# Kernel optimization log

Measured on AMD Instinct MI355X. Metric: run time of the kernel, lower is better.

The kernel has to match this reference:

```python
import jax, jax.numpy as jnp
import numpy as np

N_NODES = 100000
N_EDGES = 3200000
HIDDEN = 64
OUT = 1


def setup_inputs() -> dict:
    key = jax.random.key(0)
    k_z, k_e, k_w1, k_b1, k_w2, k_b2 = jax.random.split(key, 6)
    z = jax.random.normal(k_z, (N_NODES, HIDDEN), dtype=jnp.float32)
    edge_index = jax.random.randint(k_e, (2, N_EDGES), 0, N_NODES, dtype=jnp.int64)
    # torch Linear default init: U(-1/sqrt(fan_in), 1/sqrt(fan_in))
    lim1 = 1.0 / np.sqrt(2 * HIDDEN)
    lim2 = 1.0 / np.sqrt(HIDDEN)
    W1 = jax.random.uniform(k_w1, (2 * HIDDEN, HIDDEN), jnp.float32, -lim1, lim1)
    b1 = jax.random.uniform(k_b1, (HIDDEN,), jnp.float32, -lim1, lim1)
    W2 = jax.random.uniform(k_w2, (HIDDEN, OUT), jnp.float32, -lim2, lim2)
    b2 = jax.random.uniform(k_b2, (OUT,), jnp.float32, -lim2, lim2)
    return {"z": z, "edge_index": edge_index, "W1": W1, "b1": b1, "W2": W2, "b2": b2}


def reference(z, edge_index, W1, b1, W2, b2):
    row, col = edge_index[0], edge_index[1]
    # gather + concat: [E, 2*HIDDEN]
    h = jnp.concatenate([z[row], z[col]], axis=-1)
    h = jax.nn.relu(h @ W1 + b1)   # [E, HIDDEN]
    out = h @ W2 + b2              # [E, OUT]
    return out
```

## Files before the change

### kernel.cpp

```cpp
#include <hip/hip_runtime.h>
#include <hip/hip_bf16.h>

#define HID 64

__device__ __forceinline__ float bf2f(unsigned short x) {
    return __uint_as_float(((unsigned int)x) << 16);
}

__device__ __forceinline__ unsigned short f2bf(float f) {
    unsigned int u = __float_as_uint(f);
    unsigned int r = (u + 0x7FFFu + ((u >> 16) & 1u)) >> 16;
    return (unsigned short)r;
}

__global__ __launch_bounds__(256) void node_proj_kernel(
    const float* __restrict__ z, const float* __restrict__ W1,
    const float* __restrict__ b1,
    unsigned short* __restrict__ A, unsigned short* __restrict__ B,
    int n_nodes)
{
    const int tid    = blockIdx.x * blockDim.x + threadIdx.x;
    const int lane   = tid & 63;
    const int wave   = tid >> 6;
    const int nwaves = (gridDim.x * blockDim.x) >> 6;
    const int half   = wave & 1;
    const int pair   = wave >> 1;
    const int npairs = nwaves >> 1;

    float w[HID];
#pragma unroll
    for (int k = 0; k < HID; ++k)
        w[k] = W1[(half * HID + k) * HID + lane];
    const float bias = half ? b1[lane] : 0.0f;
    unsigned short* __restrict__ dst = half ? B : A;

    for (int n = pair; n < n_nodes; n += npairs) {
        const int nu = __builtin_amdgcn_readfirstlane(n);
        const float* __restrict__ zr = z + (size_t)nu * HID;
        float a0 = bias, a1 = 0.f, a2 = 0.f, a3 = 0.f;
#pragma unroll
        for (int k4 = 0; k4 < HID / 4; ++k4) {
            a0 = fmaf(zr[4 * k4 + 0], w[4 * k4 + 0], a0);
            a1 = fmaf(zr[4 * k4 + 1], w[4 * k4 + 1], a1);
            a2 = fmaf(zr[4 * k4 + 2], w[4 * k4 + 2], a2);
            a3 = fmaf(zr[4 * k4 + 3], w[4 * k4 + 3], a3);
        }
        dst[(size_t)nu * HID + lane] = f2bf((a0 + a1) + (a2 + a3));
    }
}

__global__ __launch_bounds__(256) void edge_kernel(
    const int* __restrict__ row, const int* __restrict__ col,
    const unsigned short* __restrict__ A, const unsigned short* __restrict__ B,
    const float* __restrict__ W2, const float* __restrict__ b2,
    float* __restrict__ out, int E)
{
    const int tid    = blockIdx.x * blockDim.x + threadIdx.x;
    const int lane   = tid & 63;
    const int gwave  = tid >> 6;
    const int nwaves = (gridDim.x * blockDim.x) >> 6;
    const int sub    = lane >> 3;
    const int l8     = lane & 7;

    float w2r[8];
#pragma unroll
    for (int i = 0; i < 8; ++i) w2r[i] = W2[l8 * 8 + i];
    const float b2v = b2[0];

    const int nchunks = E >> 6;
    for (int ch = gwave; ch < nchunks; ch += nwaves) {
        const int ebase = ch << 6;
        const int r = row[ebase + lane];
        const int c = col[ebase + lane];

        uint4 av[8], bv[8];
#pragma unroll
        for (int g = 0; g < 8; ++g) {
            const int ri = __shfl(r, g * 8 + sub);
            const int ci = __shfl(c, g * 8 + sub);
            av[g] = *(const uint4*)(A + (size_t)ri * HID + l8 * 8);
            bv[g] = *(const uint4*)(B + (size_t)ci * HID + l8 * 8);
        }

#pragma unroll
        for (int g = 0; g < 8; ++g) {
            const unsigned int* au = (const unsigned int*)&av[g];
            const unsigned int* bu = (const unsigned int*)&bv[g];
            float acc = 0.f;
#pragma unroll
            for (int i = 0; i < 4; ++i) {
                float alo = __uint_as_float(au[i] << 16);
                float ahi = __uint_as_float(au[i] & 0xffff0000u);
                float blo = __uint_as_float(bu[i] << 16);
                float bhi = __uint_as_float(bu[i] & 0xffff0000u);
                float slo = fmaxf(alo + blo, 0.f);
                float shi = fmaxf(ahi + bhi, 0.f);
                acc = fmaf(slo, w2r[2 * i + 0], acc);
                acc = fmaf(shi, w2r[2 * i + 1], acc);
            }
            acc += __shfl_xor(acc, 4);
            acc += __shfl_xor(acc, 2);
            acc += __shfl_xor(acc, 1);
            if (l8 == 0) out[ebase + g * 8 + sub] = acc + b2v;
        }
    }
}

extern "C" void kernel_launch(void* const* d_in, const int* in_sizes, int n_in,
                              void* d_out, int out_size, void* d_ws, size_t ws_size,
                              hipStream_t stream) {
    const float* z  = (const float*)d_in[0];
    const int*   ei = (const int*)d_in[1];
    const float* W1 = (const float*)d_in[2];
    const float* b1 = (const float*)d_in[3];
    const float* W2 = (const float*)d_in[4];
    const float* b2 = (const float*)d_in[5];
    float* out = (float*)d_out;

    const int n_nodes = in_sizes[0] / HID;
    const int E       = in_sizes[1] / 2;
    const int* row = ei;
    const int* col = ei + E;

    unsigned short* A = (unsigned short*)d_ws;
    unsigned short* B = A + (size_t)n_nodes * HID;

    node_proj_kernel<<<2048, 256, 0, stream>>>(z, W1, b1, A, B, n_nodes);
    edge_kernel<<<2048, 256, 0, stream>>>(row, col, A, B, W2, b2, out, E);
}
```

Measured before the change: 235.9 us.

## Restructure node projection: node-per-lane with LDS-staged z and transposed W1

```diff
diff --git a/kernel.cpp b/kernel.cpp
--- a/kernel.cpp
+++ b/kernel.cpp
@@ -2,50 +2,77 @@
 #include <hip/hip_bf16.h>
 
 #define HID 64
+#define TPAD 68
 
-__device__ __forceinline__ float bf2f(unsigned short x) {
-    return __uint_as_float(((unsigned int)x) << 16);
+__device__ __forceinline__ unsigned int pack2bf(float lo, float hi) {
+    unsigned int ul = __float_as_uint(lo), uh = __float_as_uint(hi);
+    unsigned int rl = (ul + 0x7fffu + ((ul >> 16) & 1u)) >> 16;
+    unsigned int rh = (uh + 0x7fffu + ((uh >> 16) & 1u)) & 0xffff0000u;
+    return rl | rh;
 }
 
-__device__ __forceinline__ unsigned short f2bf(float f) {
-    unsigned int u = __float_as_uint(f);
-    unsigned int r = (u + 0x7FFFu + ((u >> 16) & 1u)) >> 16;
-    return (unsigned short)r;
+__global__ __launch_bounds__(256) void transpose_w1_kernel(
+    const float* __restrict__ W1, float* __restrict__ W1T)
+{
+    const int t = blockIdx.x * 256 + threadIdx.x;
+    const int h = t >> 12, j = (t >> 6) & 63, k = t & 63;
+    W1T[t] = W1[(h * HID + k) * HID + j];
 }
 
 __global__ __launch_bounds__(256) void node_proj_kernel(
-    const float* __restrict__ z, const float* __restrict__ W1,
+    const float* __restrict__ z, const float* __restrict__ W1T,
     const float* __restrict__ b1,
     unsigned short* __restrict__ A, unsigned short* __restrict__ B,
     int n_nodes)
 {
-    const int tid    = blockIdx.x * blockDim.x + threadIdx.x;
-    const int lane   = tid & 63;
-    const int wave   = tid >> 6;
-    const int nwaves = (gridDim.x * blockDim.x) >> 6;
-    const int half   = wave & 1;
-    const int pair   = wave >> 1;
-    const int npairs = nwaves >> 1;
+    __shared__ float lds[128 * TPAD];
+    const int t    = threadIdx.x;
+    const int lane = t & 63;
+    const int wv   = __builtin_amdgcn_readfirstlane(t >> 6);
+    const int base = blockIdx.x * 128;
 
-    float w[HID];
 #pragma unroll
-    for (int k = 0; k < HID; ++k)
-        w[k] = W1[(half * HID + k) * HID + lane];
-    const float bias = half ? b1[lane] : 0.0f;
-    unsigned short* __restrict__ dst = half ? B : A;
+    for (int i = 0; i < 8; ++i) {
+        const int flat = t + i * 256;
+        const int row = flat >> 4, c4 = flat & 15;
+        int gr = base + row;
+        if (gr >= n_nodes) gr = n_nodes - 1;
+        const float4 v = *(const float4*)(z + (size_t)gr * HID + c4 * 4);
+        *(float4*)(lds + row * TPAD + c4 * 4) = v;
+    }
+    __syncthreads();
 
-    for (int n = pair; n < n_nodes; n += npairs) {
-        const int nu = __builtin_amdgcn_readfirstlane(n);
-        const float* __restrict__ zr = z + (size_t)nu * HID;
-        float a0 = bias, a1 = 0.f, a2 = 0.f, a3 = 0.f;
+    const int nrow = ((wv >> 1) << 6) | lane;
+    float zr[HID];
 #pragma unroll
-        for (int k4 = 0; k4 < HID / 4; ++k4) {
-            a0 = fmaf(zr[4 * k4 + 0], w[4 * k4 + 0], a0);
-            a1 = fmaf(zr[4 * k4 + 1], w[4 * k4 + 1], a1);
-            a2 = fmaf(zr[4 * k4 + 2], w[4 * k4 + 2], a2);
-            a3 = fmaf(zr[4 * k4 + 3], w[4 * k4 + 3], a3);
+    for (int k4 = 0; k4 < 16; ++k4) {
+        const float4 v = *(const float4*)(lds + nrow * TPAD + k4 * 4);
+        zr[4 * k4 + 0] = v.x; zr[4 * k4 + 1] = v.y;
+        zr[4 * k4 + 2] = v.z; zr[4 * k4 + 3] = v.w;
+    }
+
+    const int hsel = wv & 1;
+    const float* __restrict__ wbase = W1T + (hsel << 12);
+    unsigned short* __restrict__ dstbase = hsel ? B : A;
+    const int node = base + nrow;
+    const bool ok = node < n_nodes;
+    unsigned int* __restrict__ drow = (unsigned int*)(dstbase + (size_t)node * HID);
+
+    for (int j = 0; j < HID; j += 2) {
+        const float* __restrict__ w0 = wbase + j * HID;
+        const float* __restrict__ w1 = w0 + HID;
+        float a0 = hsel ? b1[j]     : 0.0f;
+        float b0 = hsel ? b1[j + 1] : 0.0f;
+        float a1 = 0.0f, b1v = 0.0f;
+#pragma unroll
+        for (int k = 0; k < HID; k += 2) {
+            a0  = fmaf(zr[k],     w0[k],     a0);
+            a1  = fmaf(zr[k + 1], w0[k + 1], a1);
+            b0  = fmaf(zr[k],     w1[k],     b0);
+            b1v = fmaf(zr[k + 1], w1[k + 1], b1v);
         }
-        dst[(size_t)nu * HID + lane] = f2bf((a0 + a1) + (a2 + a3));
+        const unsigned int p = pack2bf(a0 + a1, b0 + b1v);
+        if (ok) drow[j >> 1] = p;
     }
 }
 
@@ -124,7 +151,10 @@
 
     unsigned short* A = (unsigned short*)d_ws;
     unsigned short* B = A + (size_t)n_nodes * HID;
+    float* W1T = (float*)(B + (size_t)n_nodes * HID);
 
-    node_proj_kernel<<<2048, 256, 0, stream>>>(z, W1, b1, A, B, n_nodes);
+    transpose_w1_kernel<<<32, 256, 0, stream>>>(W1, W1T);
+    const int nblocks = (n_nodes + 127) / 128;
+    node_proj_kernel<<<nblocks, 256, 0, stream>>>(z, W1T, b1, A, B, n_nodes);
     edge_kernel<<<2048, 256, 0, stream>>>(row, col, A, B, W2, b2, out, E);
 }
```

Result: slower. 282.5 us (+19.8%).

## Use MFMA for node projection and split edge pass into two half-width passes

Applied to the files above, without the earlier changes.

```diff
diff --git a/kernel.cpp b/kernel.cpp
--- a/kernel.cpp
+++ b/kernel.cpp
@@ -2,6 +2,9 @@
 #include <hip/hip_bf16.h>
 
 #define HID 64
+
+typedef __attribute__((ext_vector_type(8))) short bf16x8;
+typedef __attribute__((ext_vector_type(4))) float f32x4;
 
 __device__ __forceinline__ float bf2f(unsigned short x) {
     return __uint_as_float(((unsigned int)x) << 16);
@@ -9,77 +12,117 @@
 
 __device__ __forceinline__ unsigned short f2bf(float f) {
     unsigned int u = __float_as_uint(f);
-    unsigned int r = (u + 0x7FFFu + ((u >> 16) & 1u)) >> 16;
-    return (unsigned short)r;
+    return (unsigned short)((u + 0x7fffu + ((u >> 16) & 1u)) >> 16);
 }
 
-__global__ __launch_bounds__(256) void node_proj_kernel(
-    const float* __restrict__ z, const float* __restrict__ W1,
+__device__ __forceinline__ unsigned int pack2bf(float lo, float hi) {
+    unsigned int ul = __float_as_uint(lo), uh = __float_as_uint(hi);
+    unsigned int rl = (ul + 0x7fffu + ((ul >> 16) & 1u)) >> 16;
+    unsigned int rh = (uh + 0x7fffu + ((uh >> 16) & 1u)) & 0xffff0000u;
+    return rl | rh;
+}
+
+__global__ __launch_bounds__(256) void prep_weights(
+    const float* __restrict__ W1, unsigned short* __restrict__ W1bt)
+{
+    const int t = blockIdx.x * 256 + threadIdx.x;
+    const int c = t >> 6, k = t & 63;
+    W1bt[t] = f2bf(W1[(((c >> 6) << 6) + k) * HID + (c & 63)]);
+}
+
+__global__ __launch_bounds__(256) void node_proj_mfma(
+    const float* __restrict__ z, const unsigned short* __restrict__ W1bt,
     const float* __restrict__ b1,
-    unsigned short* __restrict__ A, unsigned short* __restrict__ B,
-    int n_nodes)
+    unsigned short* __restrict__ A0, unsigned short* __restrict__ A1,
+    unsigned short* __restrict__ B0, unsigned short* __restrict__ B1,
+    int n_tiles)
 {
-    const int tid    = blockIdx.x * blockDim.x + threadIdx.x;
-    const int lane   = tid & 63;
-    const int wave   = tid >> 6;
-    const int nwaves = (gridDim.x * blockDim.x) >> 6;
-    const int half   = wave & 1;
-    const int pair   = wave >> 1;
-    const int npairs = nwaves >> 1;
+    const int tid  = blockIdx.x * 256 + threadIdx.x;
+    const int lane = tid & 63;
+    const int wv   = tid >> 6;
+    const int nw   = (gridDim.x * 256) >> 6;
+    const int q    = lane >> 4;
+    const int r    = lane & 15;
 
-    float w[HID];
+    bf16x8 wf[8][2];
 #pragma unroll
-    for (int k = 0; k < HID; ++k)
-        w[k] = W1[(half * HID + k) * HID + lane];
-    const float bias = half ? b1[lane] : 0.0f;
-    unsigned short* __restrict__ dst = half ? B : A;
+    for (int ct = 0; ct < 8; ++ct)
+#pragma unroll
+        for (int ks = 0; ks < 2; ++ks)
+            wf[ct][ks] = *(const bf16x8*)(W1bt + (ct * 16 + r) * HID + ks * 32 + q * 8);
 
-    for (int n = pair; n < n_nodes; n += npairs) {
-        const int nu = __builtin_amdgcn_readfirstlane(n);
-        const float* __restrict__ zr = z + (size_t)nu * HID;
-        float a0 = bias, a1 = 0.f, a2 = 0.f, a3 = 0.f;
+    float bias[4];
 #pragma unroll
-        for (int k4 = 0; k4 < HID / 4; ++k4) {
-            a0 = fmaf(zr[4 * k4 + 0], w[4 * k4 + 0], a0);
-            a1 = fmaf(zr[4 * k4 + 1], w[4 * k4 + 1], a1);
-            a2 = fmaf(zr[4 * k4 + 2], w[4 * k4 + 2], a2);
-            a3 = fmaf(zr[4 * k4 + 3], w[4 * k4 + 3], a3);
+    for (int i = 0; i < 4; ++i) bias[i] = b1[i * 16 + r];
+
+    unsigned short* const dsts[8] = {A0, A0, A1, A1, B0, B0, B1, B1};
+
+    for (int t = wv; t < n_tiles; t += nw) {
+        const int rowb = t * 16;
+        const float* zb = z + (size_t)(rowb + r) * HID;
+
+        bf16x8 af[2];
+#pragma unroll
+        for (int ks = 0; ks < 2; ++ks) {
+            const float4 f0 = *(const float4*)(zb + ks * 32 + q * 8);
+            const float4 f1 = *(const float4*)(zb + ks * 32 + q * 8 + 4);
+            unsigned int u[4];
+            u[0] = pack2bf(f0.x, f0.y); u[1] = pack2bf(f0.z, f0.w);
+            u[2] = pack2bf(f1.x, f1.y); u[3] = pack2bf(f1.z, f1.w);
+            af[ks] = *(bf16x8*)u;
         }
-        dst[(size_t)nu * HID + lane] = f2bf((a0 + a1) + (a2 + a3));
+
+#pragma unroll
+        for (int ct = 0; ct < 8; ++ct) {
+            f32x4 acc = {0.f, 0.f, 0.f, 0.f};
+            acc = __builtin_amdgcn_mfma_f32_16x16x32_bf16(af[0], wf[ct][0], acc, 0, 0, 0);
+            acc = __builtin_amdgcn_mfma_f32_16x16x32_bf16(af[1], wf[ct][1], acc, 0, 0, 0);
+            const float bv = (ct >= 4) ? bias[ct - 4] : 0.0f;
+            unsigned short* __restrict__ dst = dsts[ct];
+            const int colw = (ct & 1) * 16 + r;
+#pragma unroll
+            for (int j = 0; j < 4; ++j) {
+                const int node = rowb + q * 4 + j;
+                dst[(size_t)node * 32 + colw] = f2bf(acc[j] + bv);
+            }
+        }
     }
 }
 
-__global__ __launch_bounds__(256) void edge_kernel(
+template <int PASS>
+__global__ __launch_bounds__(256) void edge_half_kernel(
     const int* __restrict__ row, const int* __restrict__ col,
-    const unsigned short* __restrict__ A, const unsigned short* __restrict__ B,
+    const unsigned short* __restrict__ XA, const unsigned short* __restrict__ XB,
     const float* __restrict__ W2, const float* __restrict__ b2,
-    float* __restrict__ out, int E)
+    float* __restrict__ out, int nchunks)
 {
-    const int tid    = blockIdx.x * blockDim.x + threadIdx.x;
-    const int lane   = tid & 63;
-    const int gwave  = tid >> 6;
-    const int nwaves = (gridDim.x * blockDim.x) >> 6;
-    const int sub    = lane >> 3;
-    const int l8     = lane & 7;
+    const int tid  = blockIdx.x * 256 + threadIdx.x;
+    const int lane = tid & 63;
+    const int wv   = tid >> 6;
+    const int nw   = (gridDim.x * 256) >> 6;
+    const int sub  = lane >> 2;
+    const int l4   = lane & 3;
 
     float w2r[8];
 #pragma unroll
-    for (int i = 0; i < 8; ++i) w2r[i] = W2[l8 * 8 + i];
+    for (int i = 0; i < 8; ++i) w2r[i] = W2[PASS * 32 + l4 * 8 + i];
     const float b2v = b2[0];
 
-    const int nchunks = E >> 6;
-    for (int ch = gwave; ch < nchunks; ch += nwaves) {
-        const int ebase = ch << 6;
-        const int r = row[ebase + lane];
-        const int c = col[ebase + lane];
+    for (int ch = wv; ch < nchunks; ch += nw) {
+        const int ebase = ch << 7;
+        const int r0 = row[ebase + lane],      c0 = col[ebase + lane];
+        const int r1 = row[ebase + 64 + lane], c1 = col[ebase + 64 + lane];
+        float o0 = 0.f, o1 = 0.f;
+        if (PASS == 1) { o0 = out[ebase + lane]; o1 = out[ebase + 64 + lane]; }
 
         uint4 av[8], bv[8];
 #pragma unroll
         for (int g = 0; g < 8; ++g) {
-            const int ri = __shfl(r, g * 8 + sub);
-            const int ci = __shfl(c, g * 8 + sub);
-            av[g] = *(const uint4*)(A + (size_t)ri * HID + l8 * 8);
-            bv[g] = *(const uint4*)(B + (size_t)ci * HID + l8 * 8);
+            const int e  = (g & 3) * 16 + sub;
+            const int ri = (g < 4) ? __shfl(r0, e) : __shfl(r1, e);
+            const int ci = (g < 4) ? __shfl(c0, e) : __shfl(c1, e);
+            av[g] = *(const uint4*)(XA + (size_t)ri * 32 + l4 * 8);
+            bv[g] = *(const uint4*)(XB + (size_t)ci * 32 + l4 * 8);
         }
 
 #pragma unroll
@@ -93,15 +136,15 @@
                 float ahi = __uint_as_float(au[i] & 0xffff0000u);
                 float blo = __uint_as_float(bu[i] << 16);
                 float bhi = __uint_as_float(bu[i] & 0xffff0000u);
-                float slo = fmaxf(alo + blo, 0.f);
-                float shi = fmaxf(ahi + bhi, 0.f);
-                acc = fmaf(slo, w2r[2 * i + 0], acc);
-                acc = fmaf(shi, w2r[2 * i + 1], acc);
+                acc = fmaf(fmaxf(alo + blo, 0.f), w2r[2 * i + 0], acc);
+                acc = fmaf(fmaxf(ahi + bhi, 0.f), w2r[2 * i + 1], acc);
             }
-            acc += __shfl_xor(acc, 4);
+            acc += __shfl_xor(acc, 1);
             acc += __shfl_xor(acc, 2);
-            acc += __shfl_xor(acc, 1);
-            if (l8 == 0) out[ebase + g * 8 + sub] = acc + b2v;
+            const int eo   = (g & 3) * 16 + sub;
+            const float bs = (PASS == 0) ? b2v
+                             : ((g < 4) ? __shfl(o0, eo) : __shfl(o1, eo));
+            if (l4 == 0) out[ebase + ((g < 4) ? 0 : 64) + eo] = acc + bs;
         }
     }
 }
@@ -122,9 +165,16 @@
     const int* row = ei;
     const int* col = ei + E;
 
-    unsigned short* A = (unsigned short*)d_ws;
-    unsigned short* B = A + (size_t)n_nodes * HID;
+    const size_t arr = (size_t)n_nodes * 32;
+    unsigned short* A0 = (unsigned short*)d_ws;
+    unsigned short* A1 = A0 + arr;
+    unsigned short* B0 = A1 + arr;
+    unsigned short* B1 = B0 + arr;
+    unsigned short* W1bt = B1 + arr;
 
-    node_proj_kernel<<<2048, 256, 0, stream>>>(z, W1, b1, A, B, n_nodes);
-    edge_kernel<<<2048, 256, 0, stream>>>(row, col, A, B, W2, b2, out, E);
+    prep_weights<<<32, 256, 0, stream>>>(W1, W1bt);
+    node_proj_mfma<<<256, 256, 0, stream>>>(z, W1bt, b1, A0, A1, B0, B1, n_nodes / 16);
+    const int nchunks = E >> 7;
+    edge_half_kernel<0><<<2048, 256, 0, stream>>>(row, col, A0, B0, W2, b2, out, nchunks);
+    edge_half_kernel<1><<<2048, 256, 0, stream>>>(row, col, A1, B1, W2, b2, out, nchunks);
 }
```

After: 268.4 us. 1.14x slower.
